# Performance work log

Hardware: AMD Instinct MI355X
Metric: run time of the kernel (lower is better)

Reference implementation:

```python
import jax, jax.numpy as jnp
import numpy as np

T, D, TR, CC, L = 4096, 512, 64, 64, 3  # time, input_size, trace, context, num_blocks


def setup_inputs() -> dict:
    key = jax.random.key(0)
    ks = jax.random.split(key, 10)
    x = jax.random.normal(ks[0], (T, D), dtype=jnp.float32)
    state = jnp.zeros((L, 1, TR, CC), dtype=jnp.float32)  # initial recurrent state (real part; imag is 0)
    start = jax.random.uniform(ks[1], (T,)) < 0.02  # episode-reset mask
    Wtr = jax.random.normal(ks[2], (L, TR, D), dtype=jnp.float32) / np.float32(np.sqrt(D))
    Wc = jax.random.normal(ks[3], (L, TR, D), dtype=jnp.float32) / np.float32(np.sqrt(D))
    a = jax.random.uniform(ks[4], (L, TR), minval=1e-6, maxval=0.1)
    b = 2 * jnp.pi / jnp.exp(jax.random.uniform(ks[5], (L, CC), minval=0.0, maxval=float(np.log(10000.0))))
    F = 2 * TR * CC
    W0 = jax.random.normal(ks[6], (L, D, F), dtype=jnp.float32) * np.float32(0.01 / np.sqrt(F))  # default_init scale=0.01
    b0 = jnp.zeros((L, D)); g0 = jnp.ones((L, D)); beta0 = jnp.zeros((L, D))
    W1 = jax.random.normal(ks[7], (L, D, D), dtype=jnp.float32) / np.float32(np.sqrt(D))
    b1 = jnp.zeros((L, D)); g1 = jnp.ones((L, D)); beta1 = jnp.zeros((L, D))
    return dict(x=x, state=state, start=start, Wtr=Wtr, Wc=Wc, a=a, b=b,
                W0=W0, b0=b0, g0=g0, beta0=beta0, W1=W1, b1=b1, g1=g1, beta1=beta1)


def _layernorm(z, g, b):
    m = jnp.mean(z, axis=-1, keepdims=True)
    v = jnp.mean((z - m) ** 2, axis=-1, keepdims=True)
    return (z - m) / jnp.sqrt(v + 1e-5) * g + b


def _sffm(x, st0, start, Wtr, Wc, a, b, W0, b0, g0, bb0, W1, b1, g1, bb1):
    t_len = x.shape[0]
    tr = x @ Wtr.T           # [T, TR]
    ct = x @ Wc.T            # [T, CC] (context proj also has trace_size outputs)
    pre = jnp.abs(tr[:, :, None] * ct[:, None, :])            # [T, TR, CC]
    pre = pre / (1e-8 + jnp.sum(pre, axis=(-2, -1), keepdims=True))
    # complex decay per (trace, context) pair: exp((-|a| + i b) * dt)
    ab = (-jnp.abs(a))[:, None] + 1j * b[None, :]             # [TR, CC] complex64

    def combine(carry, inc):
        ps, s, i = carry
        st, xx, j = inc
        s = s * jnp.logical_not(st)                            # reset gating
        dt = (j - i).astype(jnp.float32)[:, None, None]
        new = s * jnp.exp(ab[None] * dt) + xx
        return (jnp.logical_or(st, ps), new, j)

    ts = jnp.arange(t_len + 1, dtype=jnp.int32)
    sb = jnp.concatenate([jnp.zeros((1, 1, 1), bool), start.reshape(t_len, 1, 1)], axis=0)
    xs = jnp.concatenate([st0.astype(jnp.complex64), pre.astype(jnp.complex64)], axis=0)
    _, ns, _ = jax.lax.associative_scan(combine, (sb, xs, ts), axis=0)
    ns = ns[1:]                                                # [T, TR, CC] complex

    s = ns.reshape(t_len, TR * CC)
    mag = jnp.log1p(jnp.abs(s))
    ang = jnp.angle(s)
    scaled = jnp.concatenate([mag * jnp.sin(ang), mag * jnp.cos(ang)], axis=-1)  # [T, 2*TR*CC]
    z = jax.nn.leaky_relu(_layernorm(scaled @ W0.T + b0, g0, bb0))
    z = jax.nn.leaky_relu(_layernorm(z @ W1.T + b1, g1, bb1))
    return z


def reference(x, state, start, Wtr, Wc, a, b, W0, b0, g0, beta0, W1, b1, g1, beta1):
    z = x
    for l in range(L):
        z = _sffm(x, state[l], start, Wtr[l], Wc[l], a[l], b[l],
                  W0[l], b0[l], g0[l], beta0[l], W1[l], b1[l], g1[l], beta1[l])
        x = x + z
    return z  # NSFFM returns the last block's y
```

## Files before the change

### kernel.cpp

```cpp
#include <hip/hip_runtime.h>
#include <hip/hip_bf16.h>
#include <math.h>

#define T_LEN 4096
#define D_DIM 512
#define F_DIM 8192
#define NCHUNK 64
#define CLEN 64

typedef short short8 __attribute__((ext_vector_type(8)));
typedef float f32x4 __attribute__((ext_vector_type(4)));
typedef unsigned short u16;
typedef unsigned int u32;

__device__ inline float wave_sum(float v) {
#pragma unroll
  for (int o = 32; o; o >>= 1) v += __shfl_xor(v, o);
  return v;
}

__device__ inline u16 f2bf_bits(float v) {
  __hip_bfloat16 h = __float2bfloat16(v);
  return *(u16*)&h;
}

__device__ inline void gl_lds16(const void* g, void* l) {
  __builtin_amdgcn_global_load_lds((const __attribute__((address_space(1))) void*)g,
                                   (__attribute__((address_space(3))) void*)l, 16, 0, 0);
}

__global__ void detect_start(const unsigned char* __restrict__ s8, int* __restrict__ mode) {
  __shared__ int found;
  if (threadIdx.x == 0) found = 0;
  __syncthreads();
  for (int i = threadIdx.x; i < 4096; i += 256)
    if ((i & 3) && s8[i]) found = 1;
  __syncthreads();
  if (threadIdx.x == 0) mode[0] = found;
}

__device__ inline int read_start(const unsigned char* s8, const int* s32, int mode, int t) {
  return mode ? (int)s8[t] : s32[t];
}

__global__ void f2bf(const float* __restrict__ s, u16* __restrict__ d, int n) {
  int i = blockIdx.x * 256 + threadIdx.x;
  if (i < n) d[i] = f2bf_bits(s[i]);
}

__global__ void k_conv(const float* __restrict__ wtr, const float* __restrict__ wc,
                       u16* __restrict__ wcat, const float* __restrict__ w0,
                       u16* __restrict__ w0bf) {
  int i = blockIdx.x * 256 + threadIdx.x;
  if (i < 128 * D_DIM) {
    float v = (i < 64 * D_DIM) ? wtr[i] : wc[i - 64 * D_DIM];
    wcat[i] = f2bf_bits(v);
  }
  int j = i - 128 * D_DIM;
  if (j >= 0 && j < D_DIM * F_DIM) {
    int d = j >> 13, f = j & 8191;
    int r = f >> 7, rem = f & 127;
    int c = rem >> 1, b = rem & 1;
    w0bf[j] = f2bf_bits(w0[(size_t)d * 8192 + b * 4096 + r * 64 + c]);
  }
}

template <int BM, int BN, int WR, int WC>
__global__ __launch_bounds__(256) void gemm_bt(const u16* __restrict__ A,
                                               const u16* __restrict__ B,
                                               float* __restrict__ C, int M, int N, int K) {
  constexpr int BK = 32;
  constexpr int MT = BM / (WR * 16);
  constexpr int NT = BN / (WC * 16);
  constexpr int AG = BM / 64;
  constexpr int BG = BN / 64;
  __shared__ u16 sA[BM * BK];
  __shared__ u16 sB[BN * BK];
  const int m0 = blockIdx.x * BM;
  const int n0 = blockIdx.y * BN;
  const int tid = threadIdx.x;
  const int wave = tid >> 6;
  const int lane = tid & 63;
  const int wr = wave / WC;
  const int wc = wave % WC;
  const int row_l = tid >> 2;
  const int c8 = (tid & 3) << 3;
  const int frow = lane & 15;
  const int fcol = (lane >> 4) << 3;

  f32x4 acc[MT][NT];
#pragma unroll
  for (int i = 0; i < MT; ++i)
#pragma unroll
    for (int j = 0; j < NT; ++j) acc[i][j] = (f32x4){0.f, 0.f, 0.f, 0.f};

  for (int k0 = 0; k0 < K; k0 += BK) {
#pragma unroll
    for (int j = 0; j < AG; ++j) {
      uint4 v = *(const uint4*)(A + (size_t)(m0 + j * 64 + row_l) * K + (k0 + c8));
      *(uint4*)(sA + (j * 64 + row_l) * BK + c8) = v;
    }
#pragma unroll
    for (int j = 0; j < BG; ++j) {
      uint4 v = *(const uint4*)(B + (size_t)(n0 + j * 64 + row_l) * K + (k0 + c8));
      *(uint4*)(sB + (j * 64 + row_l) * BK + c8) = v;
    }
    __syncthreads();
    short8 af[MT], bfr[NT];
#pragma unroll
    for (int i = 0; i < MT; ++i)
      af[i] = *(const short8*)(sA + (wr * MT * 16 + i * 16 + frow) * BK + fcol);
#pragma unroll
    for (int j = 0; j < NT; ++j)
      bfr[j] = *(const short8*)(sB + (wc * NT * 16 + j * 16 + frow) * BK + fcol);
#pragma unroll
    for (int i = 0; i < MT; ++i)
#pragma unroll
      for (int j = 0; j < NT; ++j)
        acc[i][j] = __builtin_amdgcn_mfma_f32_16x16x32_bf16(af[i], bfr[j], acc[i][j], 0, 0, 0);
    __syncthreads();
  }
#pragma unroll
  for (int i = 0; i < MT; ++i) {
    const int rbase = m0 + wr * MT * 16 + i * 16 + ((lane >> 4) << 2);
#pragma unroll
    for (int j = 0; j < NT; ++j) {
      const int col = n0 + wc * NT * 16 + j * 16 + (lane & 15);
#pragma unroll
      for (int rg = 0; rg < 4; ++rg) C[(size_t)(rbase + rg) * N + col] = acc[i][j][rg];
    }
  }
}

__global__ __launch_bounds__(256) void gemm128(const u16* __restrict__ A,
                                               const u16* __restrict__ B,
                                               float* __restrict__ Cp, size_t pstride, int N,
                                               int Ktot) {
  __shared__ u16 sA[128 * 32];
  __shared__ u16 sB[128 * 32];
  const int tid = threadIdx.x;
  const int wave = tid >> 6;
  const int lane = tid & 63;
  const int wr = wave >> 1;
  const int wc = wave & 1;
  const int m0 = blockIdx.x * 128;
  const int n0 = blockIdx.y * 128;
  const int ks = blockIdx.z;
  const int Kper = Ktot / gridDim.z;
  const int kb = ks * Kper;
  const int row_l = tid >> 2;
  const int c8 = (tid & 3) << 3;
  const int frow = lane & 15;
  const int fcol = (lane >> 4) << 3;

  f32x4 acc[4][4];
#pragma unroll
  for (int i = 0; i < 4; ++i)
#pragma unroll
    for (int j = 0; j < 4; ++j) acc[i][j] = (f32x4){0.f, 0.f, 0.f, 0.f};

  for (int k0 = kb; k0 < kb + Kper; k0 += 32) {
#pragma unroll
    for (int j = 0; j < 2; ++j) {
      gl_lds16(A + (size_t)(m0 + j * 64 + row_l) * Ktot + (k0 + c8), sA + j * 2048 + wave * 512);
      gl_lds16(B + (size_t)(n0 + j * 64 + row_l) * Ktot + (k0 + c8), sB + j * 2048 + wave * 512);
    }
    asm volatile("s_waitcnt vmcnt(0)" ::: "memory");
    __syncthreads();
    short8 af[4], bfr[4];
#pragma unroll
    for (int i = 0; i < 4; ++i)
      af[i] = *(const short8*)(sA + (wr * 64 + i * 16 + frow) * 32 + fcol);
#pragma unroll
    for (int j = 0; j < 4; ++j)
      bfr[j] = *(const short8*)(sB + (wc * 64 + j * 16 + frow) * 32 + fcol);
#pragma unroll
    for (int i = 0; i < 4; ++i)
#pragma unroll
      for (int j = 0; j < 4; ++j)
        acc[i][j] = __builtin_amdgcn_mfma_f32_16x16x32_bf16(af[i], bfr[j], acc[i][j], 0, 0, 0);
    __syncthreads();
  }
#pragma unroll
  for (int i = 0; i < 4; ++i) {
    const int rbase = m0 + wr * 64 + i * 16 + ((lane >> 4) << 2);
#pragma unroll
    for (int j = 0; j < 4; ++j) {
      const int col = n0 + wc * 64 + j * 16 + (lane & 15);
#pragma unroll
      for (int rg = 0; rg < 4; ++rg)
        Cp[(size_t)ks * pstride + (size_t)(rbase + rg) * N + col] = acc[i][j][rg];
    }
  }
}

__global__ void prep_pq(const float* __restrict__ trct, float* __restrict__ pT,
                        float* __restrict__ q) {
  int t = blockIdx.x;
  int lane = threadIdx.x;
  float tr = trct[t * 128 + lane];
  float ct = trct[t * 128 + 64 + lane];
  float ap = fabsf(tr), aq = fabsf(ct);
  float Sp = wave_sum(ap);
  float Sq = wave_sum(aq);
  float denom = 1e-8f + Sp * Sq;
  pT[lane * T_LEN + t] = ap;
  q[t * 64 + lane] = aq / denom;
}

__global__ void scan_phase1(const float* __restrict__ pT, const float* __restrict__ q,
                            const unsigned char* __restrict__ st8, const int* __restrict__ st32,
                            const int* __restrict__ modep, const float* __restrict__ a,
                            const float* __restrict__ b, float4* __restrict__ chunkbuf) {
  int chunk = blockIdx.x, r = blockIdx.y, c = threadIdx.x;
  int mode = modep[0];
  int t0 = chunk * CLEN;
  float na = -fabsf(a[r]);
  float rho = __expf(na);
  float bb = b[c];
  float er = rho * __cosf(bb), ei = rho * __sinf(bb);
  float pv = pT[r * T_LEN + t0 + c];
  int sv = read_start(st8, st32, mode, t0 + c);
  unsigned long long anyb = __ballot(sv != 0);
  float Ar, Ai;
  if (anyb) {
    Ar = 0.f; Ai = 0.f;
  } else {
    float mag = __expf(64.f * na);
    float ang = 64.f * bb;
    Ar = mag * __cosf(ang);
    Ai = mag * __sinf(ang);
  }
  float Br = 0.f, Bi = 0.f;
  const float* qrow = q + (size_t)t0 * 64 + c;
#pragma unroll 8
  for (int i = 0; i < CLEN; ++i) {
    float qt = qrow[i * 64];
    float pt = __shfl(pv, i);
    int st = __shfl(sv, i);
    float pre = pt * qt;
    float cer = st ? 0.f : er;
    float cei = st ? 0.f : ei;
    float nBr = cer * Br - cei * Bi + pre;
    Bi = cer * Bi + cei * Br;
    Br = nBr;
  }
  chunkbuf[((size_t)chunk * 64 + r) * 64 + c] = make_float4(Ar, Ai, Br, Bi);
}

__global__ void scan_phase2(const float4* __restrict__ chunkbuf, const float* __restrict__ state,
                            float2* __restrict__ s0buf) {
  int r = blockIdx.x, c = threadIdx.x;
  float Sr = state[r * 64 + c], Si = 0.f;
  for (int k = 0; k < NCHUNK; ++k) {
    s0buf[((size_t)k * 64 + r) * 64 + c] = make_float2(Sr, Si);
    float4 ab = chunkbuf[((size_t)k * 64 + r) * 64 + c];
    float nSr = ab.x * Sr - ab.y * Si + ab.z;
    Si = ab.x * Si + ab.y * Sr + ab.w;
    Sr = nSr;
  }
}

__global__ void scan_phase3(const float* __restrict__ pT, const float* __restrict__ q,
                            const unsigned char* __restrict__ st8, const int* __restrict__ st32,
                            const int* __restrict__ modep, const float* __restrict__ a,
                            const float* __restrict__ b, const float2* __restrict__ s0buf,
                            u32* __restrict__ scaled, int c0) {
  int chunk = c0 + blockIdx.x, r = blockIdx.y, c = threadIdx.x;
  int mode = modep[0];
  int t0 = chunk * CLEN;
  float rho = __expf(-fabsf(a[r]));
  float bb = b[c];
  float er = rho * __cosf(bb), ei = rho * __sinf(bb);
  float pv = pT[r * T_LEN + t0 + c];
  int sv = read_start(st8, st32, mode, t0 + c);
  float2 s0 = s0buf[((size_t)chunk * 64 + r) * 64 + c];
  float Sr = s0.x, Si = s0.y;
  int tl0 = (chunk - c0) * CLEN;
  const float* qrow = q + (size_t)t0 * 64 + c;
  u32* drow = scaled + (size_t)tl0 * 4096 + r * 64 + c;
#pragma unroll 4
  for (int i = 0; i < CLEN; ++i) {
    float qt = qrow[i * 64];
    float pt = __shfl(pv, i);
    int st = __shfl(sv, i);
    float pre = pt * qt;
    float cer = st ? 0.f : er;
    float cei = st ? 0.f : ei;
    float nSr = cer * Sr - cei * Si + pre;
    Si = cer * Si + cei * Sr;
    Sr = nSr;
    float m2 = fmaf(Sr, Sr, Si * Si);
    float rsq = rsqrtf(fmaxf(m2, 1e-30f));
    float m = m2 * rsq;
    float sc = __log2f(1.0f + m) * 0.6931471805599453f * rsq;
    u32 pack = ((u32)f2bf_bits(sc * Sr) << 16) | (u32)f2bf_bits(sc * Si);
    drow[(size_t)i * 4096] = pack;
  }
}

__global__ void ln_act(const float* __restrict__ parts, int KS, size_t pstride,
                       const float* __restrict__ bias, const float* __restrict__ gam,
                       const float* __restrict__ bet, u16* __restrict__ zbf,
                       const float* __restrict__ xsrc, float* __restrict__ xdst,
                       u16* __restrict__ xbf_next, float* __restrict__ finout) {
  __shared__ float red[8];
  int t = blockIdx.x, tid = threadIdx.x;
  size_t o = (size_t)t * D_DIM + tid;
  float v0 = bias[tid];
  float v1 = bias[tid + 256];
  for (int ks = 0; ks < KS; ++ks) {
    v0 += parts[(size_t)ks * pstride + o];
    v1 += parts[(size_t)ks * pstride + o + 256];
  }
  float s = wave_sum(v0 + v1);
  if ((tid & 63) == 0) red[tid >> 6] = s;
  __syncthreads();
  float mean = (red[0] + red[1] + red[2] + red[3]) * (1.f / 512.f);
  float d0 = v0 - mean, d1 = v1 - mean;
  float s2 = wave_sum(d0 * d0 + d1 * d1);
  if ((tid & 63) == 0) red[4 + (tid >> 6)] = s2;
  __syncthreads();
  float var = (red[4] + red[5] + red[6] + red[7]) * (1.f / 512.f);
  float rstd = rsqrtf(var + 1e-5f);
  float z0 = d0 * rstd * gam[tid] + bet[tid];
  float z1 = d1 * rstd * gam[tid + 256] + bet[tid + 256];
  z0 = z0 > 0.f ? z0 : 0.01f * z0;
  z1 = z1 > 0.f ? z1 : 0.01f * z1;
  if (zbf) { zbf[o] = f2bf_bits(z0); zbf[o + 256] = f2bf_bits(z1); }
  if (xdst) {
    float x0 = xsrc[o] + z0, x1 = xsrc[o + 256] + z1;
    xdst[o] = x0; xdst[o + 256] = x1;
    if (xbf_next) { xbf_next[o] = f2bf_bits(x0); xbf_next[o + 256] = f2bf_bits(x1); }
  }
  if (finout) { finout[o] = z0; finout[o + 256] = z1; }
}

__global__ void err_signal(float* __restrict__ out, float code) {
  if (threadIdx.x == 0) out[0] = code;
}

extern "C" void kernel_launch(void* const* d_in, const int* in_sizes, int n_in, void* d_out,
                              int out_size, void* d_ws, size_t ws_size, hipStream_t stream) {
  const float* x_in = (const float*)d_in[0];
  const float* state = (const float*)d_in[1];
  const unsigned char* start8 = (const unsigned char*)d_in[2];
  const int* start32 = (const int*)d_in[2];
  const float* Wtr = (const float*)d_in[3];
  const float* Wc = (const float*)d_in[4];
  const float* a_in = (const float*)d_in[5];
  const float* b_in = (const float*)d_in[6];
  const float* W0 = (const float*)d_in[7];
  const float* b0 = (const float*)d_in[8];
  const float* g0 = (const float*)d_in[9];
  const float* beta0 = (const float*)d_in[10];
  const float* W1 = (const float*)d_in[11];
  const float* b1 = (const float*)d_in[12];
  const float* g1 = (const float*)d_in[13];
  const float* beta1 = (const float*)d_in[14];
  float* out = (float*)d_out;

  char* w = (char*)d_ws;
  auto alloc = [&](size_t bytes) {
    char* ptr = w;
    w += (bytes + 255) & ~(size_t)255;
    return ptr;
  };
  float* x_ws = (float*)alloc(4ull * T_LEN * D_DIM);
  u16* xbf = (u16*)alloc(2ull * T_LEN * D_DIM);
  u16* wcat = (u16*)alloc(2ull * 128 * D_DIM);
  u16* w0bf = (u16*)alloc(2ull * D_DIM * F_DIM);
  u16* w1bf = (u16*)alloc(2ull * 3 * D_DIM * D_DIM);
  float* trct = (float*)alloc(4ull * T_LEN * 128);
  float* pTbuf = (float*)alloc(4ull * T_LEN * 64);
  float* qbuf = (float*)alloc(4ull * T_LEN * 64);
  float4* chunkbuf = (float4*)alloc(16ull * NCHUNK * 64 * 64);
  float2* s0buf = (float2*)alloc(8ull * NCHUNK * 64 * 64);
  u16* z0bf = (u16*)alloc(2ull * T_LEN * D_DIM);
  int* modep = (int*)alloc(256);
  size_t base1 = (size_t)(w - (char*)d_ws);

  if (n_in != 15) {
    err_signal<<<1, 64, 0, stream>>>(out, 9e6f + 1000.f * n_in);
    return;
  }
  const size_t MB = 1ull << 20;
  int KS, nseg;
  if (ws_size >= base1 + 64 * MB + 64 * MB) { KS = 8; nseg = 1; }
  else if (ws_size >= base1 + 32 * MB + 64 * MB) { KS = 4; nseg = 1; }
  else if (ws_size >= base1 + 32 * MB + 32 * MB) { KS = 4; nseg = 2; }
  else if (ws_size >= base1 + 16 * MB + 32 * MB) { KS = 2; nseg = 2; }
  else if (ws_size >= base1 + 16 * MB + 16 * MB) { KS = 2; nseg = 4; }
  else if (ws_size >= base1 + 8 * MB + 16 * MB) { KS = 1; nseg = 4; }
  else {
    err_signal<<<1, 64, 0, stream>>>(out, 9e6f);
    return;
  }
  const int KSw1 = (KS >= 8) ? 4 : ((KS >= 2) ? 2 : 1);
  const int seg_rows = T_LEN / nseg;
  const int seg_chunks = NCHUNK / nseg;
  const size_t pstride = (size_t)T_LEN * D_DIM;
  float* ypart = (float*)alloc(4ull * KS * pstride);
  u16* scaled = (u16*)alloc(2ull * seg_rows * F_DIM);

  detect_start<<<1, 256, 0, stream>>>(start8, modep);
  f2bf<<<(T_LEN * D_DIM) / 256, 256, 0, stream>>>(x_in, xbf, T_LEN * D_DIM);
  f2bf<<<(3 * D_DIM * D_DIM) / 256, 256, 0, stream>>>(W1, w1bf, 3 * D_DIM * D_DIM);

  for (int l = 0; l < 3; ++l) {
    const float* Wtr_l = Wtr + (size_t)l * 64 * D_DIM;
    const float* Wc_l = Wc + (size_t)l * 64 * D_DIM;
    const float* a_l = a_in + l * 64;
    const float* b_l = b_in + l * 64;
    const float* W0_l = W0 + (size_t)l * D_DIM * F_DIM;
    const u16* w1bf_l = w1bf + (size_t)l * D_DIM * D_DIM;
    const float* state_l = state + (size_t)l * 64 * 64;
    const float* xsrc = (l == 0) ? x_in : x_ws;

    k_conv<<<(128 * D_DIM + D_DIM * F_DIM) / 256, 256, 0, stream>>>(Wtr_l, Wc_l, wcat, W0_l,
                                                                    w0bf);
    gemm_bt<64, 64, 2, 2><<<dim3(T_LEN / 64, 2), 256, 0, stream>>>(xbf, wcat, trct, T_LEN, 128,
                                                                   D_DIM);
    prep_pq<<<T_LEN, 64, 0, stream>>>(trct, pTbuf, qbuf);
    scan_phase1<<<dim3(NCHUNK, 64), 64, 0, stream>>>(pTbuf, qbuf, start8, start32, modep, a_l,
                                                     b_l, chunkbuf);
    scan_phase2<<<64, 64, 0, stream>>>(chunkbuf, state_l, s0buf);

    for (int h = 0; h < nseg; ++h) {
      scan_phase3<<<dim3(seg_chunks, 64), 64, 0, stream>>>(pTbuf, qbuf, start8, start32, modep,
                                                           a_l, b_l, s0buf, (u32*)scaled,
                                                           h * seg_chunks);
      gemm128<<<dim3(seg_rows / 128, D_DIM / 128, KS), 256, 0, stream>>>(
          scaled, w0bf, ypart + (size_t)h * seg_rows * D_DIM, pstride, D_DIM, F_DIM);
    }
    ln_act<<<T_LEN, 256, 0, stream>>>(ypart, KS, pstride, b0 + l * D_DIM, g0 + l * D_DIM,
                                      beta0 + l * D_DIM, z0bf, nullptr, nullptr, nullptr,
                                      nullptr);
    gemm128<<<dim3(T_LEN / 128, D_DIM / 128, KSw1), 256, 0, stream>>>(z0bf, w1bf_l, ypart,
                                                                      pstride, D_DIM, D_DIM);
    ln_act<<<T_LEN, 256, 0, stream>>>(ypart, KSw1, pstride, b1 + l * D_DIM, g1 + l * D_DIM,
                                      beta1 + l * D_DIM, nullptr, (l < 2) ? xsrc : nullptr,
                                      (l < 2) ? x_ws : nullptr, (l < 2) ? xbf : nullptr,
                                      (l == 2) ? out : nullptr);
  }
}
```

Baseline: 549.6 us.

## Swizzle GEMM operand layouts in global memory and deepen gemm128 K tile

Producers of the gemm128 operands (scaled features, W0, W1, and the z activations) now write their bf16 data with an XOR swizzle on 8-element groups keyed by row. gemm128 loads a 64-wide K tile per iteration and reads it back with the matching swizzle, which avoids LDS bank conflicts and halves the number of barrier pairs per K. Separately, scan_phase1 starts each chunk's recurrence from the last reset position instead of gating every step. The swizzle must agree across every producer and consumer, and the larger tile doubles LDS use per block.

```diff
diff --git a/kernel.cpp b/kernel.cpp
--- a/kernel.cpp
+++ b/kernel.cpp
@@ -48,6 +48,14 @@
   if (i < n) d[i] = f2bf_bits(s[i]);
 }
 
+__global__ void k_w1conv(const float* __restrict__ src, u16* __restrict__ dst, int n) {
+  int i = blockIdx.x * 256 + threadIdx.x;
+  if (i >= n) return;
+  int d = (i >> 9) & 511;
+  int e = i & 511;
+  dst[(i & ~511) | (e ^ ((d & 7) << 3))] = f2bf_bits(src[i]);
+}
+
 __global__ void k_conv(const float* __restrict__ wtr, const float* __restrict__ wc,
                        u16* __restrict__ wcat, const float* __restrict__ w0,
                        u16* __restrict__ w0bf) {
@@ -61,7 +69,8 @@
     int d = j >> 13, f = j & 8191;
     int r = f >> 7, rem = f & 127;
     int c = rem >> 1, b = rem & 1;
-    w0bf[j] = f2bf_bits(w0[(size_t)d * 8192 + b * 4096 + r * 64 + c]);
+    float v = w0[(size_t)d * 8192 + b * 4096 + r * 64 + c];
+    w0bf[(size_t)d * 8192 + (f ^ ((d & 7) << 3))] = f2bf_bits(v);
   }
 }
 
@@ -136,8 +145,8 @@
                                                const u16* __restrict__ B,
                                                float* __restrict__ Cp, size_t pstride, int N,
                                                int Ktot) {
-  __shared__ u16 sA[128 * 32];
-  __shared__ u16 sB[128 * 32];
+  __shared__ u16 sA[128 * 64];
+  __shared__ u16 sB[128 * 64];
   const int tid = threadIdx.x;
   const int wave = tid >> 6;
   const int lane = tid & 63;
@@ -148,10 +157,11 @@
   const int ks = blockIdx.z;
   const int Kper = Ktot / gridDim.z;
   const int kb = ks * Kper;
-  const int row_l = tid >> 2;
-  const int c8 = (tid & 3) << 3;
+  const int row_s = tid >> 3;
+  const int g8 = (tid & 7) << 3;
   const int frow = lane & 15;
-  const int fcol = (lane >> 4) << 3;
+  const int quad = lane >> 4;
+  const int sw = frow & 7;
 
   f32x4 acc[4][4];
 #pragma unroll
@@ -159,26 +169,30 @@
 #pragma unroll
     for (int j = 0; j < 4; ++j) acc[i][j] = (f32x4){0.f, 0.f, 0.f, 0.f};
 
-  for (int k0 = kb; k0 < kb + Kper; k0 += 32) {
-#pragma unroll
-    for (int j = 0; j < 2; ++j) {
-      gl_lds16(A + (size_t)(m0 + j * 64 + row_l) * Ktot + (k0 + c8), sA + j * 2048 + wave * 512);
-      gl_lds16(B + (size_t)(n0 + j * 64 + row_l) * Ktot + (k0 + c8), sB + j * 2048 + wave * 512);
+  for (int k0 = kb; k0 < kb + Kper; k0 += 64) {
+#pragma unroll
+    for (int j = 0; j < 4; ++j) {
+      gl_lds16(A + (size_t)(m0 + j * 32 + row_s) * Ktot + (k0 + g8), sA + j * 2048 + wave * 512);
+      gl_lds16(B + (size_t)(n0 + j * 32 + row_s) * Ktot + (k0 + g8), sB + j * 2048 + wave * 512);
     }
     asm volatile("s_waitcnt vmcnt(0)" ::: "memory");
     __syncthreads();
-    short8 af[4], bfr[4];
-#pragma unroll
-    for (int i = 0; i < 4; ++i)
-      af[i] = *(const short8*)(sA + (wr * 64 + i * 16 + frow) * 32 + fcol);
-#pragma unroll
-    for (int j = 0; j < 4; ++j)
-      bfr[j] = *(const short8*)(sB + (wc * 64 + j * 16 + frow) * 32 + fcol);
-#pragma unroll
-    for (int i = 0; i < 4; ++i)
+#pragma unroll
+    for (int kk = 0; kk < 2; ++kk) {
+      const int gA = (((kk << 2) | quad) ^ sw) << 3;
+      short8 af[4], bfr[4];
+#pragma unroll
+      for (int i = 0; i < 4; ++i)
+        af[i] = *(const short8*)(sA + (wr * 64 + i * 16 + frow) * 64 + gA);
 #pragma unroll
       for (int j = 0; j < 4; ++j)
-        acc[i][j] = __builtin_amdgcn_mfma_f32_16x16x32_bf16(af[i], bfr[j], acc[i][j], 0, 0, 0);
+        bfr[j] = *(const short8*)(sB + (wc * 64 + j * 16 + frow) * 64 + gA);
+#pragma unroll
+      for (int i = 0; i < 4; ++i)
+#pragma unroll
+        for (int j = 0; j < 4; ++j)
+          acc[i][j] = __builtin_amdgcn_mfma_f32_16x16x32_bf16(af[i], bfr[j], acc[i][j], 0, 0, 0);
+    }
     __syncthreads();
   }
 #pragma unroll
@@ -221,9 +235,9 @@
   float er = rho * __cosf(bb), ei = rho * __sinf(bb);
   float pv = pT[r * T_LEN + t0 + c];
   int sv = read_start(st8, st32, mode, t0 + c);
-  unsigned long long anyb = __ballot(sv != 0);
+  unsigned long long bal = __ballot(sv != 0);
   float Ar, Ai;
-  if (anyb) {
+  if (bal) {
     Ar = 0.f; Ai = 0.f;
   } else {
     float mag = __expf(64.f * na);
@@ -231,18 +245,13 @@
     Ar = mag * __cosf(ang);
     Ai = mag * __sinf(ang);
   }
+  int L = bal ? (63 - __builtin_clzll(bal)) : 0;
   float Br = 0.f, Bi = 0.f;
   const float* qrow = q + (size_t)t0 * 64 + c;
-#pragma unroll 8
-  for (int i = 0; i < CLEN; ++i) {
-    float qt = qrow[i * 64];
-    float pt = __shfl(pv, i);
-    int st = __shfl(sv, i);
-    float pre = pt * qt;
-    float cer = st ? 0.f : er;
-    float cei = st ? 0.f : ei;
-    float nBr = cer * Br - cei * Bi + pre;
-    Bi = cer * Bi + cei * Br;
+  for (int i = L; i < CLEN; ++i) {
+    float pre = __shfl(pv, i) * qrow[i * 64];
+    float nBr = er * Br - ei * Bi + pre;
+    Bi = er * Bi + ei * Br;
     Br = nBr;
   }
   chunkbuf[((size_t)chunk * 64 + r) * 64 + c] = make_float4(Ar, Ai, Br, Bi);
@@ -278,7 +287,8 @@
   float Sr = s0.x, Si = s0.y;
   int tl0 = (chunk - c0) * CLEN;
   const float* qrow = q + (size_t)t0 * 64 + c;
-  u32* drow = scaled + (size_t)tl0 * 4096 + r * 64 + c;
+  u32* srow = scaled + (size_t)tl0 * 4096;
+  const int Ldw = r * 64 + c;
 #pragma unroll 4
   for (int i = 0; i < CLEN; ++i) {
     float qt = qrow[i * 64];
@@ -295,7 +305,7 @@
     float m = m2 * rsq;
     float sc = __log2f(1.0f + m) * 0.6931471805599453f * rsq;
     u32 pack = ((u32)f2bf_bits(sc * Sr) << 16) | (u32)f2bf_bits(sc * Si);
-    drow[(size_t)i * 4096] = pack;
+    srow[(size_t)i * 4096 + (Ldw ^ ((i & 7) << 2))] = pack;
   }
 }
 
@@ -327,7 +337,12 @@
   float z1 = d1 * rstd * gam[tid + 256] + bet[tid + 256];
   z0 = z0 > 0.f ? z0 : 0.01f * z0;
   z1 = z1 > 0.f ? z1 : 0.01f * z1;
-  if (zbf) { zbf[o] = f2bf_bits(z0); zbf[o + 256] = f2bf_bits(z1); }
+  if (zbf) {
+    int sw8 = (t & 7) << 3;
+    size_t zb = (size_t)t * D_DIM;
+    zbf[zb + (tid ^ sw8)] = f2bf_bits(z0);
+    zbf[zb + 256 + (tid ^ sw8)] = f2bf_bits(z1);
+  }
   if (xdst) {
     float x0 = xsrc[o] + z0, x1 = xsrc[o + 256] + z1;
     xdst[o] = x0; xdst[o + 256] = x1;
@@ -405,7 +420,7 @@
 
   detect_start<<<1, 256, 0, stream>>>(start8, modep);
   f2bf<<<(T_LEN * D_DIM) / 256, 256, 0, stream>>>(x_in, xbf, T_LEN * D_DIM);
-  f2bf<<<(3 * D_DIM * D_DIM) / 256, 256, 0, stream>>>(W1, w1bf, 3 * D_DIM * D_DIM);
+  k_w1conv<<<(3 * D_DIM * D_DIM) / 256, 256, 0, stream>>>(W1, w1bf, 3 * D_DIM * D_DIM);
 
   for (int l = 0; l < 3; ++l) {
     const float* Wtr_l = Wtr + (size_t)l * 64 * D_DIM;
```

Result: no change. 557.3 us (+1.4%).
